# Kernel optimization log

Measured on AMD Instinct MI355X. Metric: run time of the kernel, lower is better.

The kernel has to match this reference:

```python
import jax, jax.numpy as jnp
import numpy as np

# Shapes: [n_boxes, batch, ch, H, W] as produced by Uncropper in the original module.
N_BOXES, BATCH, CH_KQ, CH_V, H, W = 32, 4, 64, 64, 80, 80


def setup_inputs() -> dict:
    key = jax.random.key(0)
    k1, k2, k3 = jax.random.split(key, 3)
    q_big = jax.random.normal(k1, (N_BOXES, BATCH, CH_KQ, H, W), dtype=jnp.float32)
    k_big = jax.random.normal(k2, (N_BOXES, BATCH, CH_KQ, H, W), dtype=jnp.float32)
    v_big = jax.random.normal(k3, (N_BOXES, BATCH, CH_V, H, W), dtype=jnp.float32)
    return {"q_big": q_big, "k_big": k_big, "v_big": v_big}


def reference(q_big, k_big, v_big):
    # Original loop: for i in range(n_boxes):
    #   w = softmax(sum(q_big[i] * k_big, dim=-3, keepdim=True) / sqrt(ch_kq), dim=-5)
    #   delta_big[i] = sum(w * v_big, dim=-5)
    # Vectorized: attention over the box axis, independent per (batch, h, w) pixel.
    scale = 1.0 / np.sqrt(q_big.shape[2]).astype(np.float32)
    # scores[i, j, b, h, w] = <q_big[i, b, :, h, w], k_big[j, b, :, h, w]>
    scores = jnp.einsum('ibchw,jbchw->ijbhw', q_big, k_big) * scale
    w = jax.nn.softmax(scores, axis=1)  # softmax over source box j (dim=-5 in torch)
    delta_big = jnp.einsum('ijbhw,jbchw->ibchw', w, v_big)
    return delta_big
```

## Files before the change

kernel.cpp:

```cpp
#include <hip/hip_runtime.h>


#define NBOX    32
#define NBATCH  4
#define CH      64
#define HW      6400
#define PIX     16
#define CC      4
#define NCHUNK  (CH / CC)
#define IB      2
#define NT      256
#define LPJ     36
#define NTILES  (HW / PIX)
#define NUNITS  (NBATCH * NTILES)
#define CSTRIDE ((size_t)CC * HW)

#define SYNC() do { __builtin_amdgcn_sched_barrier(0); __syncthreads(); \
                    __builtin_amdgcn_sched_barrier(0); } while (0)

__global__ __launch_bounds__(NT, 2)
void box_attn_kernel(const float* __restrict__ q,
                     const float* __restrict__ k,
                     const float* __restrict__ v,
                     float* __restrict__ out) {
    __shared__ float lds[2][CC * PIX * LPJ];

    const int t   = threadIdx.x;
    const int bid = blockIdx.x;
    const int unit = (bid & 7) * (NUNITS / 8) + (bid >> 3);
    const int b    = unit / NTILES;
    const int p0   = (unit % NTILES) * PIX;

    const int pp = t & (PIX - 1);
    const int i0 = (t >> 4) * IB;

    const int pg = t & 3;
    const int jj = (t >> 2) & 31;
    const int cs = t >> 7;
    const size_t g0 = ((size_t)(jj * NBATCH + b) * CH + cs) * HW + p0 + pg * 4;
    const size_t gd = (size_t)2 * HW;
    const int    l0 = (cs * PIX + pg * 4) * LPJ + jj;
    const int    ld = 2 * PIX * LPJ;

    const size_t qoff0 = ((size_t)((i0 + 0) * NBATCH + b) * CH) * HW + p0 + pp;
    const size_t qoff1 = ((size_t)((i0 + 1) * NBATCH + b) * CH) * HW + p0 + pp;

    float s0[NBOX], s1[NBOX];
#pragma unroll
    for (int j = 0; j < NBOX; ++j) { s0[j] = 0.f; s1[j] = 0.f; }

    float4 rb0, rb1;

    rb0 = *reinterpret_cast<const float4*>(k + g0);
    rb1 = *reinterpret_cast<const float4*>(k + g0 + gd);
    {
        float* d0 = &lds[0][l0];
        d0[0] = rb0.x; d0[LPJ] = rb0.y; d0[2 * LPJ] = rb0.z; d0[3 * LPJ] = rb0.w;
        float* d1 = &lds[0][l0 + ld];
        d1[0] = rb1.x; d1[LPJ] = rb1.y; d1[2 * LPJ] = rb1.z; d1[3 * LPJ] = rb1.w;
    }
    float qf0[CC], qf1[CC], qn0[CC], qn1[CC];
#pragma unroll
    for (int c = 0; c < CC; ++c) {
        qf0[c] = q[qoff0 + (size_t)c * HW];
        qf1[c] = q[qoff1 + (size_t)c * HW];
    }
    SYNC();

#pragma unroll 1
    for (int ch = 0; ch < NCHUNK; ++ch) {
        const bool pre = (ch + 1 < NCHUNK);
        if (pre) {
            const float* src = k + g0 + (size_t)(ch + 1) * CSTRIDE;
            rb0 = *reinterpret_cast<const float4*>(src);
            rb1 = *reinterpret_cast<const float4*>(src + gd);
#pragma unroll
            for (int c = 0; c < CC; ++c) {
                qn0[c] = q[qoff0 + (size_t)((ch + 1) * CC + c) * HW];
                qn1[c] = q[qoff1 + (size_t)((ch + 1) * CC + c) * HW];
            }
        }

        const float* buf = &lds[ch & 1][0];
#pragma unroll
        for (int c = 0; c < CC; ++c) {
            const float* row = &buf[(c * PIX + pp) * LPJ];
#pragma unroll
            for (int jg = 0; jg < 8; ++jg) {
                float4 kv = *reinterpret_cast<const float4*>(row + jg * 4);
                s0[jg * 4 + 0] = fmaf(qf0[c], kv.x, s0[jg * 4 + 0]);
                s0[jg * 4 + 1] = fmaf(qf0[c], kv.y, s0[jg * 4 + 1]);
                s0[jg * 4 + 2] = fmaf(qf0[c], kv.z, s0[jg * 4 + 2]);
                s0[jg * 4 + 3] = fmaf(qf0[c], kv.w, s0[jg * 4 + 3]);
                s1[jg * 4 + 0] = fmaf(qf1[c], kv.x, s1[jg * 4 + 0]);
                s1[jg * 4 + 1] = fmaf(qf1[c], kv.y, s1[jg * 4 + 1]);
                s1[jg * 4 + 2] = fmaf(qf1[c], kv.z, s1[jg * 4 + 2]);
                s1[jg * 4 + 3] = fmaf(qf1[c], kv.w, s1[jg * 4 + 3]);
            }
        }

        if (pre) {
            float* d0 = &lds[(ch + 1) & 1][l0];
            d0[0] = rb0.x; d0[LPJ] = rb0.y; d0[2 * LPJ] = rb0.z; d0[3 * LPJ] = rb0.w;
            float* d1 = &lds[(ch + 1) & 1][l0 + ld];
            d1[0] = rb1.x; d1[LPJ] = rb1.y; d1[2 * LPJ] = rb1.z; d1[3 * LPJ] = rb1.w;
        }
        SYNC();
        if (pre) {
#pragma unroll
            for (int c = 0; c < CC; ++c) { qf0[c] = qn0[c]; qf1[c] = qn1[c]; }
        }
    }

    rb0 = *reinterpret_cast<const float4*>(v + g0);
    rb1 = *reinterpret_cast<const float4*>(v + g0 + gd);
    {
        float m = s0[0];
#pragma unroll
        for (int j = 1; j < NBOX; ++j) m = fmaxf(m, s0[j]);
        float sum = 0.f;
#pragma unroll
        for (int j = 0; j < NBOX; ++j) { float e = __expf((s0[j] - m) * 0.125f); s0[j] = e; sum += e; }
        float inv = 1.f / sum;
#pragma unroll
        for (int j = 0; j < NBOX; ++j) s0[j] *= inv;
    }
    {
        float m = s1[0];
#pragma unroll
        for (int j = 1; j < NBOX; ++j) m = fmaxf(m, s1[j]);
        float sum = 0.f;
#pragma unroll
        for (int j = 0; j < NBOX; ++j) { float e = __expf((s1[j] - m) * 0.125f); s1[j] = e; sum += e; }
        float inv = 1.f / sum;
#pragma unroll
        for (int j = 0; j < NBOX; ++j) s1[j] *= inv;
    }

    float4 rA0, rA1, rB0, rB1;
    {
        float* d0 = &lds[0][l0];
        d0[0] = rb0.x; d0[LPJ] = rb0.y; d0[2 * LPJ] = rb0.z; d0[3 * LPJ] = rb0.w;
        float* d1 = &lds[0][l0 + ld];
        d1[0] = rb1.x; d1[LPJ] = rb1.y; d1[2 * LPJ] = rb1.z; d1[3 * LPJ] = rb1.w;
    }
    {
        const float* src = v + g0 + CSTRIDE;
        rA0 = *reinterpret_cast<const float4*>(src);
        rA1 = *reinterpret_cast<const float4*>(src + gd);
    }
    SYNC();

#pragma unroll 1
    for (int ch = 0; ch < NCHUNK; ++ch) {
        if (ch + 2 < NCHUNK) {
            const float* src = v + g0 + (size_t)(ch + 2) * CSTRIDE;
            rB0 = *reinterpret_cast<const float4*>(src);
            rB1 = *reinterpret_cast<const float4*>(src + gd);
        }

        float acc0[CC], acc1[CC];
#pragma unroll
        for (int c = 0; c < CC; ++c) { acc0[c] = 0.f; acc1[c] = 0.f; }

        const float* buf = &lds[ch & 1][0];
#pragma unroll
        for (int c = 0; c < CC; ++c) {
            const float* row = &buf[(c * PIX + pp) * LPJ];
#pragma unroll
            for (int jg = 0; jg < 8; ++jg) {
                float4 vv = *reinterpret_cast<const float4*>(row + jg * 4);
                acc0[c] = fmaf(s0[jg * 4 + 0], vv.x, acc0[c]);
                acc0[c] = fmaf(s0[jg * 4 + 1], vv.y, acc0[c]);
                acc0[c] = fmaf(s0[jg * 4 + 2], vv.z, acc0[c]);
                acc0[c] = fmaf(s0[jg * 4 + 3], vv.w, acc0[c]);
                acc1[c] = fmaf(s1[jg * 4 + 0], vv.x, acc1[c]);
                acc1[c] = fmaf(s1[jg * 4 + 1], vv.y, acc1[c]);
                acc1[c] = fmaf(s1[jg * 4 + 2], vv.z, acc1[c]);
                acc1[c] = fmaf(s1[jg * 4 + 3], vv.w, acc1[c]);
            }
        }
#pragma unroll
        for (int c = 0; c < CC; ++c) {
            out[qoff0 + (size_t)(ch * CC + c) * HW] = acc0[c];
            out[qoff1 + (size_t)(ch * CC + c) * HW] = acc1[c];
        }

        if (ch + 1 < NCHUNK) {
            float* d0 = &lds[(ch + 1) & 1][l0];
            d0[0] = rA0.x; d0[LPJ] = rA0.y; d0[2 * LPJ] = rA0.z; d0[3 * LPJ] = rA0.w;
            float* d1 = &lds[(ch + 1) & 1][l0 + ld];
            d1[0] = rA1.x; d1[LPJ] = rA1.y; d1[2 * LPJ] = rA1.z; d1[3 * LPJ] = rA1.w;
        }
        SYNC();
        if (ch + 2 < NCHUNK) { rA0 = rB0; rA1 = rB1; }
    }
}

extern "C" void kernel_launch(void* const* d_in, const int* in_sizes, int n_in,
                              void* d_out, int out_size, void* d_ws, size_t ws_size,
                              hipStream_t stream) {
    const float* q = (const float*)d_in[0];
    const float* k = (const float*)d_in[1];
    const float* v = (const float*)d_in[2];
    float* o = (float*)d_out;
    dim3 grid(NUNITS);
    box_attn_kernel<<<grid, NT, 0, stream>>>(q, k, v, o);
}
```

Measured before the change: 216.1 us.

## Split box-j dimension across thread pairs with 512-thread blocks and shuffle reductions

Doubles the block to 512 threads and splits the 32 source boxes between two lanes 16 apart, so each thread holds 16 score registers per query box instead of 32. Softmax max and sum and the V accumulation are combined across the lane pair with xor shuffles, and each lane stores half the output channels. Global-to-LDS staging now uses one float4 per thread per chunk with a two-deep register prefetch for K. The aim is lower register pressure and higher occupancy (launch bounds 3), at the cost of extra shuffles and twice as many LDS reads per unit of work.

```diff
diff --git a/kernel.cpp b/kernel.cpp
--- a/kernel.cpp
+++ b/kernel.cpp
@@ -8,8 +8,7 @@
 #define PIX     16
 #define CC      4
 #define NCHUNK  (CH / CC)
-#define IB      2
-#define NT      256
+#define NT      512
 #define LPJ     36
 #define NTILES  (HW / PIX)
 #define NUNITS  (NBATCH * NTILES)
@@ -18,7 +17,7 @@
 #define SYNC() do { __builtin_amdgcn_sched_barrier(0); __syncthreads(); \
                     __builtin_amdgcn_sched_barrier(0); } while (0)
 
-__global__ __launch_bounds__(NT, 2)
+__global__ __launch_bounds__(NT, 3)
 void box_attn_kernel(const float* __restrict__ q,
                      const float* __restrict__ k,
                      const float* __restrict__ v,
@@ -31,49 +30,46 @@
     const int b    = unit / NTILES;
     const int p0   = (unit % NTILES) * PIX;
 
-    const int pp = t & (PIX - 1);
-    const int i0 = (t >> 4) * IB;
+    const int pp = t & 15;
+    const int jg = (t >> 4) & 1;
+    const int ig = t >> 5;
+    const int i0 = ig * 2;
+    const int jbase = jg * 16;
 
     const int pg = t & 3;
     const int jj = (t >> 2) & 31;
     const int cs = t >> 7;
     const size_t g0 = ((size_t)(jj * NBATCH + b) * CH + cs) * HW + p0 + pg * 4;
-    const size_t gd = (size_t)2 * HW;
     const int    l0 = (cs * PIX + pg * 4) * LPJ + jj;
-    const int    ld = 2 * PIX * LPJ;
 
     const size_t qoff0 = ((size_t)((i0 + 0) * NBATCH + b) * CH) * HW + p0 + pp;
     const size_t qoff1 = ((size_t)((i0 + 1) * NBATCH + b) * CH) * HW + p0 + pp;
 
-    float s0[NBOX], s1[NBOX];
-#pragma unroll
-    for (int j = 0; j < NBOX; ++j) { s0[j] = 0.f; s1[j] = 0.f; }
-
-    float4 rb0, rb1;
-
-    rb0 = *reinterpret_cast<const float4*>(k + g0);
-    rb1 = *reinterpret_cast<const float4*>(k + g0 + gd);
-    {
-        float* d0 = &lds[0][l0];
-        d0[0] = rb0.x; d0[LPJ] = rb0.y; d0[2 * LPJ] = rb0.z; d0[3 * LPJ] = rb0.w;
-        float* d1 = &lds[0][l0 + ld];
-        d1[0] = rb1.x; d1[LPJ] = rb1.y; d1[2 * LPJ] = rb1.z; d1[3 * LPJ] = rb1.w;
-    }
+    float s0[16], s1[16];
+#pragma unroll
+    for (int j = 0; j < 16; ++j) { s0[j] = 0.f; s1[j] = 0.f; }
+
+    float4 r0, rA, rB;
     float qf0[CC], qf1[CC], qn0[CC], qn1[CC];
+
+    r0 = *reinterpret_cast<const float4*>(k + g0);
+    rA = *reinterpret_cast<const float4*>(k + g0 + CSTRIDE);
 #pragma unroll
     for (int c = 0; c < CC; ++c) {
         qf0[c] = q[qoff0 + (size_t)c * HW];
         qf1[c] = q[qoff1 + (size_t)c * HW];
     }
+    {
+        float* d = &lds[0][l0];
+        d[0] = r0.x; d[LPJ] = r0.y; d[2 * LPJ] = r0.z; d[3 * LPJ] = r0.w;
+    }
     SYNC();
 
 #pragma unroll 1
     for (int ch = 0; ch < NCHUNK; ++ch) {
-        const bool pre = (ch + 1 < NCHUNK);
-        if (pre) {
-            const float* src = k + g0 + (size_t)(ch + 1) * CSTRIDE;
-            rb0 = *reinterpret_cast<const float4*>(src);
-            rb1 = *reinterpret_cast<const float4*>(src + gd);
+        if (ch + 2 < NCHUNK)
+            rB = *reinterpret_cast<const float4*>(k + g0 + (size_t)(ch + 2) * CSTRIDE);
+        if (ch + 1 < NCHUNK) {
 #pragma unroll
             for (int c = 0; c < CC; ++c) {
                 qn0[c] = q[qoff0 + (size_t)((ch + 1) * CC + c) * HW];
@@ -84,80 +80,72 @@
         const float* buf = &lds[ch & 1][0];
 #pragma unroll
         for (int c = 0; c < CC; ++c) {
-            const float* row = &buf[(c * PIX + pp) * LPJ];
-#pragma unroll
-            for (int jg = 0; jg < 8; ++jg) {
-                float4 kv = *reinterpret_cast<const float4*>(row + jg * 4);
-                s0[jg * 4 + 0] = fmaf(qf0[c], kv.x, s0[jg * 4 + 0]);
-                s0[jg * 4 + 1] = fmaf(qf0[c], kv.y, s0[jg * 4 + 1]);
-                s0[jg * 4 + 2] = fmaf(qf0[c], kv.z, s0[jg * 4 + 2]);
-                s0[jg * 4 + 3] = fmaf(qf0[c], kv.w, s0[jg * 4 + 3]);
-                s1[jg * 4 + 0] = fmaf(qf1[c], kv.x, s1[jg * 4 + 0]);
-                s1[jg * 4 + 1] = fmaf(qf1[c], kv.y, s1[jg * 4 + 1]);
-                s1[jg * 4 + 2] = fmaf(qf1[c], kv.z, s1[jg * 4 + 2]);
-                s1[jg * 4 + 3] = fmaf(qf1[c], kv.w, s1[jg * 4 + 3]);
+            const float* row = &buf[(c * PIX + pp) * LPJ + jbase];
+#pragma unroll
+            for (int o = 0; o < 4; ++o) {
+                float4 kv = *reinterpret_cast<const float4*>(row + o * 4);
+                s0[o * 4 + 0] = fmaf(qf0[c], kv.x, s0[o * 4 + 0]);
+                s0[o * 4 + 1] = fmaf(qf0[c], kv.y, s0[o * 4 + 1]);
+                s0[o * 4 + 2] = fmaf(qf0[c], kv.z, s0[o * 4 + 2]);
+                s0[o * 4 + 3] = fmaf(qf0[c], kv.w, s0[o * 4 + 3]);
+                s1[o * 4 + 0] = fmaf(qf1[c], kv.x, s1[o * 4 + 0]);
+                s1[o * 4 + 1] = fmaf(qf1[c], kv.y, s1[o * 4 + 1]);
+                s1[o * 4 + 2] = fmaf(qf1[c], kv.z, s1[o * 4 + 2]);
+                s1[o * 4 + 3] = fmaf(qf1[c], kv.w, s1[o * 4 + 3]);
             }
         }
 
-        if (pre) {
-            float* d0 = &lds[(ch + 1) & 1][l0];
-            d0[0] = rb0.x; d0[LPJ] = rb0.y; d0[2 * LPJ] = rb0.z; d0[3 * LPJ] = rb0.w;
-            float* d1 = &lds[(ch + 1) & 1][l0 + ld];
-            d1[0] = rb1.x; d1[LPJ] = rb1.y; d1[2 * LPJ] = rb1.z; d1[3 * LPJ] = rb1.w;
+        if (ch + 1 < NCHUNK) {
+            float* d = &lds[(ch + 1) & 1][l0];
+            d[0] = rA.x; d[LPJ] = rA.y; d[2 * LPJ] = rA.z; d[3 * LPJ] = rA.w;
         }
         SYNC();
-        if (pre) {
+        rA = rB;
+        if (ch + 1 < NCHUNK) {
 #pragma unroll
             for (int c = 0; c < CC; ++c) { qf0[c] = qn0[c]; qf1[c] = qn1[c]; }
         }
     }
 
-    rb0 = *reinterpret_cast<const float4*>(v + g0);
-    rb1 = *reinterpret_cast<const float4*>(v + g0 + gd);
+    r0 = *reinterpret_cast<const float4*>(v + g0);
+    rA = *reinterpret_cast<const float4*>(v + g0 + CSTRIDE);
     {
         float m = s0[0];
 #pragma unroll
-        for (int j = 1; j < NBOX; ++j) m = fmaxf(m, s0[j]);
+        for (int j = 1; j < 16; ++j) m = fmaxf(m, s0[j]);
+        m = fmaxf(m, __shfl_xor(m, 16, 64));
         float sum = 0.f;
 #pragma unroll
-        for (int j = 0; j < NBOX; ++j) { float e = __expf((s0[j] - m) * 0.125f); s0[j] = e; sum += e; }
+        for (int j = 0; j < 16; ++j) { float e = __expf((s0[j] - m) * 0.125f); s0[j] = e; sum += e; }
+        sum += __shfl_xor(sum, 16, 64);
         float inv = 1.f / sum;
 #pragma unroll
-        for (int j = 0; j < NBOX; ++j) s0[j] *= inv;
+        for (int j = 0; j < 16; ++j) s0[j] *= inv;
     }
     {
         float m = s1[0];
 #pragma unroll
-        for (int j = 1; j < NBOX; ++j) m = fmaxf(m, s1[j]);
+        for (int j = 1; j < 16; ++j) m = fmaxf(m, s1[j]);
+        m = fmaxf(m, __shfl_xor(m, 16, 64));
         float sum = 0.f;
 #pragma unroll
-        for (int j = 0; j < NBOX; ++j) { float e = __expf((s1[j] - m) * 0.125f); s1[j] = e; sum += e; }
+        for (int j = 0; j < 16; ++j) { float e = __expf((s1[j] - m) * 0.125f); s1[j] = e; sum += e; }
+        sum += __shfl_xor(sum, 16, 64);
         float inv = 1.f / sum;
 #pragma unroll
-        for (int j = 0; j < NBOX; ++j) s1[j] *= inv;
-    }
-
-    float4 rA0, rA1, rB0, rB1;
-    {
-        float* d0 = &lds[0][l0];
-        d0[0] = rb0.x; d0[LPJ] = rb0.y; d0[2 * LPJ] = rb0.z; d0[3 * LPJ] = rb0.w;
-        float* d1 = &lds[0][l0 + ld];
-        d1[0] = rb1.x; d1[LPJ] = rb1.y; d1[2 * LPJ] = rb1.z; d1[3 * LPJ] = rb1.w;
-    }
-    {
-        const float* src = v + g0 + CSTRIDE;
-        rA0 = *reinterpret_cast<const float4*>(src);
-        rA1 = *reinterpret_cast<const float4*>(src + gd);
+        for (int j = 0; j < 16; ++j) s1[j] *= inv;
+    }
+
+    {
+        float* d = &lds[0][l0];
+        d[0] = r0.x; d[LPJ] = r0.y; d[2 * LPJ] = r0.z; d[3 * LPJ] = r0.w;
     }
     SYNC();
 
 #pragma unroll 1
     for (int ch = 0; ch < NCHUNK; ++ch) {
-        if (ch + 2 < NCHUNK) {
-            const float* src = v + g0 + (size_t)(ch + 2) * CSTRIDE;
-            rB0 = *reinterpret_cast<const float4*>(src);
-            rB1 = *reinterpret_cast<const float4*>(src + gd);
-        }
+        if (ch + 2 < NCHUNK)
+            rB = *reinterpret_cast<const float4*>(v + g0 + (size_t)(ch + 2) * CSTRIDE);
 
         float acc0[CC], acc1[CC];
 #pragma unroll
@@ -166,34 +154,38 @@
         const float* buf = &lds[ch & 1][0];
 #pragma unroll
         for (int c = 0; c < CC; ++c) {
-            const float* row = &buf[(c * PIX + pp) * LPJ];
-#pragma unroll
-            for (int jg = 0; jg < 8; ++jg) {
-                float4 vv = *reinterpret_cast<const float4*>(row + jg * 4);
-                acc0[c] = fmaf(s0[jg * 4 + 0], vv.x, acc0[c]);
-                acc0[c] = fmaf(s0[jg * 4 + 1], vv.y, acc0[c]);
-                acc0[c] = fmaf(s0[jg * 4 + 2], vv.z, acc0[c]);
-                acc0[c] = fmaf(s0[jg * 4 + 3], vv.w, acc0[c]);
-                acc1[c] = fmaf(s1[jg * 4 + 0], vv.x, acc1[c]);
-                acc1[c] = fmaf(s1[jg * 4 + 1], vv.y, acc1[c]);
-                acc1[c] = fmaf(s1[jg * 4 + 2], vv.z, acc1[c]);
-                acc1[c] = fmaf(s1[jg * 4 + 3], vv.w, acc1[c]);
+            const float* row = &buf[(c * PIX + pp) * LPJ + jbase];
+#pragma unroll
+            for (int o = 0; o < 4; ++o) {
+                float4 vv = *reinterpret_cast<const float4*>(row + o * 4);
+                acc0[c] = fmaf(s0[o * 4 + 0], vv.x, acc0[c]);
+                acc0[c] = fmaf(s0[o * 4 + 1], vv.y, acc0[c]);
+                acc0[c] = fmaf(s0[o * 4 + 2], vv.z, acc0[c]);
+                acc0[c] = fmaf(s0[o * 4 + 3], vv.w, acc0[c]);
+                acc1[c] = fmaf(s1[o * 4 + 0], vv.x, acc1[c]);
+                acc1[c] = fmaf(s1[o * 4 + 1], vv.y, acc1[c]);
+                acc1[c] = fmaf(s1[o * 4 + 2], vv.z, acc1[c]);
+                acc1[c] = fmaf(s1[o * 4 + 3], vv.w, acc1[c]);
             }
         }
 #pragma unroll
         for (int c = 0; c < CC; ++c) {
+            acc0[c] += __shfl_xor(acc0[c], 16, 64);
+            acc1[c] += __shfl_xor(acc1[c], 16, 64);
+        }
+#pragma unroll
+        for (int cc = 0; cc < 2; ++cc) {
+            const int c = jg * 2 + cc;
             out[qoff0 + (size_t)(ch * CC + c) * HW] = acc0[c];
             out[qoff1 + (size_t)(ch * CC + c) * HW] = acc1[c];
         }
 
         if (ch + 1 < NCHUNK) {
-            float* d0 = &lds[(ch + 1) & 1][l0];
-            d0[0] = rA0.x; d0[LPJ] = rA0.y; d0[2 * LPJ] = rA0.z; d0[3 * LPJ] = rA0.w;
-            float* d1 = &lds[(ch + 1) & 1][l0 + ld];
-            d1[0] = rA1.x; d1[LPJ] = rA1.y; d1[2 * LPJ] = rA1.z; d1[3 * LPJ] = rA1.w;
+            float* d = &lds[(ch + 1) & 1][l0];
+            d[0] = rA.x; d[LPJ] = rA.y; d[2 * LPJ] = rA.z; d[3 * LPJ] = rA.w;
         }
         SYNC();
-        if (ch + 2 < NCHUNK) { rA0 = rB0; rA1 = rB1; }
+        rA = rB;
     }
 }
 
```

New measurement: 287.6 us. +33.1%, slower.

## Use single-wavefront blocks over four pixels and drop block barriers

Applied to the files above, without the earlier changes.

Shrinks each block to one 64-thread wavefront handling four pixels, so the K/V staging in LDS is shared only within a wave and all __syncthreads barriers are removed. The global prefetch of K is deepened to two chunks ahead, matching the V loop. This removes barrier stalls and lets many more independent small blocks run. In exchange it relies on intra-wave ordering of LDS writes and reads, and the launch bound of 2 may let register use limit occupancy.

```diff
diff --git a/kernel.cpp b/kernel.cpp
--- a/kernel.cpp
+++ b/kernel.cpp
@@ -5,18 +5,14 @@
 #define NBATCH  4
 #define CH      64
 #define HW      6400
-#define PIX     16
+#define PIX     4
 #define CC      4
 #define NCHUNK  (CH / CC)
-#define IB      2
-#define NT      256
+#define NT      64
 #define LPJ     36
 #define NTILES  (HW / PIX)
 #define NUNITS  (NBATCH * NTILES)
 #define CSTRIDE ((size_t)CC * HW)
-
-#define SYNC() do { __builtin_amdgcn_sched_barrier(0); __syncthreads(); \
-                    __builtin_amdgcn_sched_barrier(0); } while (0)
 
 __global__ __launch_bounds__(NT, 2)
 void box_attn_kernel(const float* __restrict__ q,
@@ -31,15 +27,14 @@
     const int b    = unit / NTILES;
     const int p0   = (unit % NTILES) * PIX;
 
-    const int pp = t & (PIX - 1);
-    const int i0 = (t >> 4) * IB;
+    const int pp = t & 3;
+    const int i0 = (t >> 2) * 2;
 
-    const int pg = t & 3;
-    const int jj = (t >> 2) & 31;
-    const int cs = t >> 7;
-    const size_t g0 = ((size_t)(jj * NBATCH + b) * CH + cs) * HW + p0 + pg * 4;
+    const int jj = t & 31;
+    const int cs = t >> 5;
+    const size_t g0 = ((size_t)(jj * NBATCH + b) * CH + cs) * HW + p0;
     const size_t gd = (size_t)2 * HW;
-    const int    l0 = (cs * PIX + pg * 4) * LPJ + jj;
+    const int    l0 = (cs * PIX) * LPJ + jj;
     const int    ld = 2 * PIX * LPJ;
 
     const size_t qoff0 = ((size_t)((i0 + 0) * NBATCH + b) * CH) * HW + p0 + pp;
@@ -49,31 +44,33 @@
 #pragma unroll
     for (int j = 0; j < NBOX; ++j) { s0[j] = 0.f; s1[j] = 0.f; }
 
-    float4 rb0, rb1;
+    float4 rA0, rA1, rB0, rB1;
+    float qf0[CC], qf1[CC], qn0[CC], qn1[CC];
 
-    rb0 = *reinterpret_cast<const float4*>(k + g0);
-    rb1 = *reinterpret_cast<const float4*>(k + g0 + gd);
     {
+        float4 r0 = *reinterpret_cast<const float4*>(k + g0);
+        float4 r1 = *reinterpret_cast<const float4*>(k + g0 + gd);
         float* d0 = &lds[0][l0];
-        d0[0] = rb0.x; d0[LPJ] = rb0.y; d0[2 * LPJ] = rb0.z; d0[3 * LPJ] = rb0.w;
+        d0[0] = r0.x; d0[LPJ] = r0.y; d0[2 * LPJ] = r0.z; d0[3 * LPJ] = r0.w;
         float* d1 = &lds[0][l0 + ld];
-        d1[0] = rb1.x; d1[LPJ] = rb1.y; d1[2 * LPJ] = rb1.z; d1[3 * LPJ] = rb1.w;
+        d1[0] = r1.x; d1[LPJ] = r1.y; d1[2 * LPJ] = r1.z; d1[3 * LPJ] = r1.w;
     }
-    float qf0[CC], qf1[CC], qn0[CC], qn1[CC];
+    rA0 = *reinterpret_cast<const float4*>(k + g0 + CSTRIDE);
+    rA1 = *reinterpret_cast<const float4*>(k + g0 + CSTRIDE + gd);
 #pragma unroll
     for (int c = 0; c < CC; ++c) {
         qf0[c] = q[qoff0 + (size_t)c * HW];
         qf1[c] = q[qoff1 + (size_t)c * HW];
     }
-    SYNC();
 
 #pragma unroll 1
     for (int ch = 0; ch < NCHUNK; ++ch) {
-        const bool pre = (ch + 1 < NCHUNK);
-        if (pre) {
-            const float* src = k + g0 + (size_t)(ch + 1) * CSTRIDE;
-            rb0 = *reinterpret_cast<const float4*>(src);
-            rb1 = *reinterpret_cast<const float4*>(src + gd);
+        if (ch + 2 < NCHUNK) {
+            const float* src = k + g0 + (size_t)(ch + 2) * CSTRIDE;
+            rB0 = *reinterpret_cast<const float4*>(src);
+            rB1 = *reinterpret_cast<const float4*>(src + gd);
+        }
+        if (ch + 1 < NCHUNK) {
 #pragma unroll
             for (int c = 0; c < CC; ++c) {
                 qn0[c] = q[qoff0 + (size_t)((ch + 1) * CC + c) * HW];
@@ -99,21 +96,27 @@
             }
         }
 
-        if (pre) {
+        if (ch + 1 < NCHUNK) {
             float* d0 = &lds[(ch + 1) & 1][l0];
-            d0[0] = rb0.x; d0[LPJ] = rb0.y; d0[2 * LPJ] = rb0.z; d0[3 * LPJ] = rb0.w;
+            d0[0] = rA0.x; d0[LPJ] = rA0.y; d0[2 * LPJ] = rA0.z; d0[3 * LPJ] = rA0.w;
             float* d1 = &lds[(ch + 1) & 1][l0 + ld];
-            d1[0] = rb1.x; d1[LPJ] = rb1.y; d1[2 * LPJ] = rb1.z; d1[3 * LPJ] = rb1.w;
-        }
-        SYNC();
-        if (pre) {
+            d1[0] = rA1.x; d1[LPJ] = rA1.y; d1[2 * LPJ] = rA1.z; d1[3 * LPJ] = rA1.w;
+            rA0 = rB0; rA1 = rB1;
 #pragma unroll
             for (int c = 0; c < CC; ++c) { qf0[c] = qn0[c]; qf1[c] = qn1[c]; }
         }
     }
 
-    rb0 = *reinterpret_cast<const float4*>(v + g0);
-    rb1 = *reinterpret_cast<const float4*>(v + g0 + gd);
+    {
+        float4 r0 = *reinterpret_cast<const float4*>(v + g0);
+        float4 r1 = *reinterpret_cast<const float4*>(v + g0 + gd);
+        float* d0 = &lds[0][l0];
+        d0[0] = r0.x; d0[LPJ] = r0.y; d0[2 * LPJ] = r0.z; d0[3 * LPJ] = r0.w;
+        float* d1 = &lds[0][l0 + ld];
+        d1[0] = r1.x; d1[LPJ] = r1.y; d1[2 * LPJ] = r1.z; d1[3 * LPJ] = r1.w;
+    }
+    rA0 = *reinterpret_cast<const float4*>(v + g0 + CSTRIDE);
+    rA1 = *reinterpret_cast<const float4*>(v + g0 + CSTRIDE + gd);
     {
         float m = s0[0];
 #pragma unroll
@@ -136,20 +139,6 @@
 #pragma unroll
         for (int j = 0; j < NBOX; ++j) s1[j] *= inv;
     }
-
-    float4 rA0, rA1, rB0, rB1;
-    {
-        float* d0 = &lds[0][l0];
-        d0[0] = rb0.x; d0[LPJ] = rb0.y; d0[2 * LPJ] = rb0.z; d0[3 * LPJ] = rb0.w;
-        float* d1 = &lds[0][l0 + ld];
-        d1[0] = rb1.x; d1[LPJ] = rb1.y; d1[2 * LPJ] = rb1.z; d1[3 * LPJ] = rb1.w;
-    }
-    {
-        const float* src = v + g0 + CSTRIDE;
-        rA0 = *reinterpret_cast<const float4*>(src);
-        rA1 = *reinterpret_cast<const float4*>(src + gd);
-    }
-    SYNC();
 
 #pragma unroll 1
     for (int ch = 0; ch < NCHUNK; ++ch) {
@@ -191,9 +180,8 @@
             d0[0] = rA0.x; d0[LPJ] = rA0.y; d0[2 * LPJ] = rA0.z; d0[3 * LPJ] = rA0.w;
             float* d1 = &lds[(ch + 1) & 1][l0 + ld];
             d1[0] = rA1.x; d1[LPJ] = rA1.y; d1[2 * LPJ] = rA1.z; d1[3 * LPJ] = rA1.w;
+            rA0 = rB0; rA1 = rB1;
         }
-        SYNC();
-        if (ch + 2 < NCHUNK) { rA0 = rB0; rA1 = rB1; }
     }
 }
 
```

New measurement: 374.9 us. 73.5% more time.
